# Kernel tuning notes

Measured on AMD Instinct MI355X. Metric: run time of the kernel, lower is better.

## Reference

```python
import jax, jax.numpy as jnp
import numpy as np

G = 5000      # n_genes (nodes)
IN = 64       # in_dim
D = 128       # embed_dims
E = 240000    # edges (before self-loops)
SLOPE = 0.2   # leakyrelu_slope (outer) and GATv2 internal negative_slope (PyG default 0.2)


def setup_inputs() -> dict:
    key = jax.random.key(0)
    ks = jax.random.split(key, 12)
    s = 0.05
    return {
        "x": jax.random.normal(ks[0], (G, IN), jnp.float32),
        "edge_index": jax.random.randint(ks[1], (2, E), 0, G, jnp.int64),
        # per-gene input linears: n_genes independent Linear(in_dim -> embed_dims)
        "W_in": jax.random.normal(ks[2], (G, IN, D), jnp.float32) * s,
        "b_in": jnp.zeros((G, D), jnp.float32),
        # GATv2Conv params (heads=1): lin_l, lin_r, att, bias
        "W_l": jax.random.normal(ks[3], (D, D), jnp.float32) * s,
        "b_l": jnp.zeros((D,), jnp.float32),
        "W_r": jax.random.normal(ks[4], (D, D), jnp.float32) * s,
        "b_r": jnp.zeros((D,), jnp.float32),
        "att": jax.random.normal(ks[5], (D,), jnp.float32) * s,
        "bias": jnp.zeros((D,), jnp.float32),
        # output MLP: Linear(D*G -> D), Linear(D -> 1)
        "W1": jax.random.normal(ks[6], (D * G, D), jnp.float32) * 0.001,
        "b1": jnp.zeros((D,), jnp.float32),
        "W2": jax.random.normal(ks[7], (D, 1), jnp.float32) * s,
        "b2": jnp.zeros((1,), jnp.float32),
    }


def _leaky(v, slope):
    return jnp.where(v >= 0, v, slope * v)


def reference(x, edge_index, W_in, b_in, W_l, b_l, W_r, b_r, att, bias, W1, b1, W2, b2):
    # per-gene linear + relu: [G, IN] x [G, IN, D] -> [G, D]
    h = jax.nn.relu(jnp.einsum("gi,gid->gd", x, W_in) + b_in)

    # GATv2Conv (heads=1, concat, add_self_loops=True)
    xl = h @ W_l + b_l  # source-side transform [G, D]
    xr = h @ W_r + b_r  # target-side transform [G, D]
    loop = jnp.arange(G, dtype=edge_index.dtype)
    src = jnp.concatenate([edge_index[0], loop])  # [E+G]
    dst = jnp.concatenate([edge_index[1], loop])

    # attention logits per edge: att . LeakyReLU(xl[src] + xr[dst])
    e = _leaky(xl[src] + xr[dst], 0.2) @ att  # [E+G]

    # segment softmax over edges sharing a destination
    m = jax.ops.segment_max(e, dst, num_segments=G)  # [G]
    w = jnp.exp(e - m[dst])
    z = jax.ops.segment_sum(w, dst, num_segments=G)  # [G]
    alpha = w / z[dst]  # every node has a self-loop, z > 0

    # scatter-aggregate weighted messages
    out = jax.ops.segment_sum(alpha[:, None] * xl[src], dst, num_segments=G) + bias  # [G, D]

    out = _leaky(out, SLOPE)
    flat = out.reshape(-1)  # [G*D]
    h1 = jax.nn.relu(flat @ W1 + b1)
    return h1 @ W2 + b2  # [1]
```

## Files before the change

### kernel.cpp

```cpp
#include <hip/hip_runtime.h>
#include <math.h>

#define G 5000
#define IN 64
#define D 128
#define E 240000
#define EG (E + G)
#define SLOPE 0.2f
#define GD (G * D)
#define CAP 128
#define NB_M 1250
#define NB_PG 1250
#define NB_H 240
#define NB_X 1250

__device__ __forceinline__ float leaky(float v) { return v >= 0.f ? v : SLOPE * v; }

__global__ __launch_bounds__(256) void k_fuseA(const float* __restrict__ x,
                                               const float* __restrict__ Win,
                                               const float* __restrict__ bin,
                                               float* __restrict__ h,
                                               const int* __restrict__ srcA,
                                               const int* __restrict__ dstA,
                                               int* __restrict__ cnt,
                                               int* __restrict__ ssrc,
                                               float* __restrict__ outz) {
    if (blockIdx.x == 0 && threadIdx.x == 0) *outz = 0.f;
    if (blockIdx.x < NB_PG) {
        int g = (blockIdx.x * 256 + threadIdx.x) >> 6;
        int lane = threadIdx.x & 63;
        if (g >= G) return;
        float xv = x[g * IN + lane];
        const float* W = Win + (size_t)g * IN * D + lane * 2;
        float2 acc = *(const float2*)(bin + g * D + lane * 2);
#pragma unroll
        for (int i = 0; i < IN; ++i) {
            float xi = __shfl(xv, i);
            float2 w2 = *(const float2*)(W + (size_t)i * D);
            acc.x = fmaf(xi, w2.x, acc.x);
            acc.y = fmaf(xi, w2.y, acc.y);
        }
        float2 o = { fmaxf(acc.x, 0.f), fmaxf(acc.y, 0.f) };
        *(float2*)(h + g * D + lane * 2) = o;
    } else {
        int base = ((blockIdx.x - NB_PG) * 256 + threadIdx.x) * 4;
        if (base >= EG) return;
        if (base + 4 <= E) {
            int4 s4 = *(const int4*)(srcA + base);
            int4 d4 = *(const int4*)(dstA + base);
            int p;
            p = atomicAdd(&cnt[d4.x], 1); if (p < CAP) ssrc[d4.x * CAP + p] = s4.x;
            p = atomicAdd(&cnt[d4.y], 1); if (p < CAP) ssrc[d4.y * CAP + p] = s4.y;
            p = atomicAdd(&cnt[d4.z], 1); if (p < CAP) ssrc[d4.z * CAP + p] = s4.z;
            p = atomicAdd(&cnt[d4.w], 1); if (p < CAP) ssrc[d4.w * CAP + p] = s4.w;
        } else {
            for (int kk = 0; kk < 4; ++kk) {
                int i = base + kk;
                if (i < EG) {
                    int s, t;
                    if (i < E) { s = srcA[i]; t = dstA[i]; }
                    else { s = i - E; t = s; }
                    int p = atomicAdd(&cnt[t], 1);
                    if (p < CAP) ssrc[t * CAP + p] = s;
                }
            }
        }
    }
}

__global__ __launch_bounds__(256) void k_xlxr3(const float* __restrict__ h,
                                               const float* __restrict__ Wl,
                                               const float* __restrict__ bl,
                                               const float* __restrict__ Wr,
                                               const float* __restrict__ br,
                                               float* __restrict__ xl,
                                               float* __restrict__ xr) {
    int g0 = blockIdx.x * 4;
    int tid = threadIdx.x;
    int half = tid >> 7;
    int col = tid & 127;
    const float* W = half ? Wr : Wl;
    const float* bb = half ? br : bl;
    float* o = half ? xr : xl;
    const float* h0p = h + (size_t)(g0 + 0) * D;
    const float* h1p = h + (size_t)(g0 + 1) * D;
    const float* h2p = h + (size_t)(g0 + 2) * D;
    const float* h3p = h + (size_t)(g0 + 3) * D;
    float b = bb[col];
    float acc0 = b, acc1 = b, acc2 = b, acc3 = b;
#pragma unroll 8
    for (int k4 = 0; k4 < 32; ++k4) {
        int k = k4 * 4;
        float4 hv0 = *(const float4*)(h0p + k);
        float4 hv1 = *(const float4*)(h1p + k);
        float4 hv2 = *(const float4*)(h2p + k);
        float4 hv3 = *(const float4*)(h3p + k);
        float w0 = W[(size_t)(k + 0) * D + col];
        float w1 = W[(size_t)(k + 1) * D + col];
        float w2 = W[(size_t)(k + 2) * D + col];
        float w3 = W[(size_t)(k + 3) * D + col];
        acc0 = fmaf(hv0.x, w0, acc0); acc0 = fmaf(hv0.y, w1, acc0);
        acc0 = fmaf(hv0.z, w2, acc0); acc0 = fmaf(hv0.w, w3, acc0);
        acc1 = fmaf(hv1.x, w0, acc1); acc1 = fmaf(hv1.y, w1, acc1);
        acc1 = fmaf(hv1.z, w2, acc1); acc1 = fmaf(hv1.w, w3, acc1);
        acc2 = fmaf(hv2.x, w0, acc2); acc2 = fmaf(hv2.y, w1, acc2);
        acc2 = fmaf(hv2.z, w2, acc2); acc2 = fmaf(hv2.w, w3, acc2);
        acc3 = fmaf(hv3.x, w0, acc3); acc3 = fmaf(hv3.y, w1, acc3);
        acc3 = fmaf(hv3.z, w2, acc3); acc3 = fmaf(hv3.w, w3, acc3);
    }
    o[(size_t)(g0 + 0) * D + col] = acc0;
    o[(size_t)(g0 + 1) * D + col] = acc1;
    o[(size_t)(g0 + 2) * D + col] = acc2;
    o[(size_t)(g0 + 3) * D + col] = acc3;
}

__global__ __launch_bounds__(256) void k_aggmlp(const int* __restrict__ cnt,
                                                const int* __restrict__ ssrc,
                                                const float* __restrict__ xl,
                                                const float* __restrict__ xr,
                                                const float* __restrict__ att,
                                                const float* __restrict__ bias,
                                                const float* __restrict__ W1,
                                                float* __restrict__ partials) {
    int wid = threadIdx.x >> 6;
    int lane = threadIdx.x & 63;
    int t = __builtin_amdgcn_readfirstlane(blockIdx.x * 4 + wid);
    __shared__ float w_lds[4][64];
    __shared__ int   s_lds[4][64];
    __shared__ float2 red[4][64];
    const float* xrt = xr + (size_t)t * D;
    int lane2 = lane * 2;
    int deg = cnt[t]; if (deg > CAP) deg = CAP;
    const int* srow = ssrc + t * CAP;
    float2 acc = { 0.f, 0.f };
    float z = 0.f;
    for (int base = 0; base < deg; base += 64) {
        int nv = deg - base; if (nv > 64) nv = 64;
        int mye = base + lane;
        int s = srow[mye < deg ? mye : deg - 1];
        const float* xls = xl + (size_t)s * D;
        float v0 = 0.f, v1 = 0.f;
#pragma unroll
        for (int dc = 0; dc < D; dc += 8) {
            float4 xa = *(const float4*)(xls + dc);
            float4 xb = *(const float4*)(xls + dc + 4);
            float4 ra = *(const float4*)(xrt + dc);
            float4 rb = *(const float4*)(xrt + dc + 4);
            float4 aa = *(const float4*)(att + dc);
            float4 ab = *(const float4*)(att + dc + 4);
            v0 = fmaf(aa.x, leaky(xa.x + ra.x), v0);
            v0 = fmaf(aa.y, leaky(xa.y + ra.y), v0);
            v0 = fmaf(aa.z, leaky(xa.z + ra.z), v0);
            v0 = fmaf(aa.w, leaky(xa.w + ra.w), v0);
            v1 = fmaf(ab.x, leaky(xb.x + rb.x), v1);
            v1 = fmaf(ab.y, leaky(xb.y + rb.y), v1);
            v1 = fmaf(ab.z, leaky(xb.z + rb.z), v1);
            v1 = fmaf(ab.w, leaky(xb.w + rb.w), v1);
        }
        float w = (lane < nv) ? expf(v0 + v1) : 0.f;
        z += w;
        w_lds[wid][lane] = w;
        s_lds[wid][lane] = s;
        for (int e = 0; e < nv; e += 4) {
            float4 w4 = *(const float4*)&w_lds[wid][e];
            int4   s4 = *(const int4*)&s_lds[wid][e];
            float2 l0 = *(const float2*)(xl + (size_t)s4.x * D + lane2);
            float2 l1 = *(const float2*)(xl + (size_t)s4.y * D + lane2);
            float2 l2 = *(const float2*)(xl + (size_t)s4.z * D + lane2);
            float2 l3 = *(const float2*)(xl + (size_t)s4.w * D + lane2);
            acc.x = fmaf(w4.x, l0.x, acc.x); acc.y = fmaf(w4.x, l0.y, acc.y);
            acc.x = fmaf(w4.y, l1.x, acc.x); acc.y = fmaf(w4.y, l1.y, acc.y);
            acc.x = fmaf(w4.z, l2.x, acc.x); acc.y = fmaf(w4.z, l2.y, acc.y);
            acc.x = fmaf(w4.w, l3.x, acc.x); acc.y = fmaf(w4.w, l3.y, acc.y);
        }
    }
#pragma unroll
    for (int off = 32; off; off >>= 1) z += __shfl_xor(z, off);
    float inv = 1.f / z;
    float2 bv = *(const float2*)(bias + lane2);
    float2 o = { leaky(acc.x * inv + bv.x), leaky(acc.y * inv + bv.y) };

    const float* W1p = W1 + (size_t)t * D * D + lane2;
    float2 m = { 0.f, 0.f };
#pragma unroll 8
    for (int dp = 0; dp < 64; ++dp) {
        float fx = __shfl(o.x, dp);
        float fy = __shfl(o.y, dp);
        float2 wa = *(const float2*)(W1p + (size_t)(2 * dp) * D);
        float2 wb = *(const float2*)(W1p + (size_t)(2 * dp + 1) * D);
        m.x = fmaf(fx, wa.x, m.x); m.y = fmaf(fx, wa.y, m.y);
        m.x = fmaf(fy, wb.x, m.x); m.y = fmaf(fy, wb.y, m.y);
    }
    red[wid][lane] = m;
    __syncthreads();
    if (wid == 0) {
        float2 s0 = red[0][lane], s1 = red[1][lane], s2 = red[2][lane], s3 = red[3][lane];
        float2 s = { s0.x + s1.x + s2.x + s3.x, s0.y + s1.y + s2.y + s3.y };
        *(float2*)(partials + (size_t)blockIdx.x * D + lane2) = s;
    }
}

__global__ __launch_bounds__(1024) void k_final8(const float* __restrict__ partials,
                                                 const float* __restrict__ b1,
                                                 const float* __restrict__ W2,
                                                 const float* __restrict__ b2,
                                                 float* __restrict__ out) {
    int tid = threadIdx.x;
    int rg = tid >> 4;
    int cl = tid & 15;
    int c = blockIdx.x * 16 + cl;
    float s = 0.f;
    for (int r = rg; r < NB_M; r += 64) s += partials[(size_t)r * D + c];
    __shared__ float red[64][16];
    red[rg][cl] = s;
    __syncthreads();
    if (tid < 128) {
        int cc = tid & 15, seg = tid >> 4;
        float t2 = red[seg * 8][cc];
        for (int m = 1; m < 8; ++m) t2 += red[seg * 8 + m][cc];
        red[seg * 8][cc] = t2;
    }
    __syncthreads();
    if (tid < 16) {
        float tot = 0.f;
        for (int m = 0; m < 8; ++m) tot += red[m * 8][tid];
        float h1 = fmaxf(tot + b1[blockIdx.x * 16 + tid], 0.f);
        red[0][tid] = h1 * W2[blockIdx.x * 16 + tid];
    }
    __syncthreads();
    if (tid == 0) {
        float o = 0.f;
        for (int m = 0; m < 16; ++m) o += red[0][m];
        if (blockIdx.x == 0) o += b2[0];
        atomicAdd(out, o);
    }
}

extern "C" void kernel_launch(void* const* d_in, const int* in_sizes, int n_in,
                              void* d_out, int out_size, void* d_ws, size_t ws_size,
                              hipStream_t stream) {
    const float* x    = (const float*)d_in[0];
    const int*   ei   = (const int*)d_in[1];
    const float* Win  = (const float*)d_in[2];
    const float* bin  = (const float*)d_in[3];
    const float* Wl   = (const float*)d_in[4];
    const float* bl   = (const float*)d_in[5];
    const float* Wr   = (const float*)d_in[6];
    const float* br   = (const float*)d_in[7];
    const float* att  = (const float*)d_in[8];
    const float* bias = (const float*)d_in[9];
    const float* W1   = (const float*)d_in[10];
    const float* b1   = (const float*)d_in[11];
    const float* W2   = (const float*)d_in[12];
    const float* b2   = (const float*)d_in[13];
    float* out = (float*)d_out;

    float* ws       = (float*)d_ws;
    float* h        = ws;
    float* xl       = h  + GD;
    float* xr       = xl + GD;
    float* partials = xr + GD;
    int*   ssrc     = (int*)(partials + (size_t)NB_M * D);
    int*   cnt      = ssrc + (size_t)G * CAP;

    const int* srcA = ei;
    const int* dstA = ei + E;

    hipMemsetAsync(cnt, 0, G * sizeof(int), stream);
    k_fuseA<<<NB_PG + NB_H, 256, 0, stream>>>(x, Win, bin, h, srcA, dstA, cnt, ssrc, out);
    k_xlxr3<<<NB_X, 256, 0, stream>>>(h, Wl, bl, Wr, br, xl, xr);
    k_aggmlp<<<NB_M, 256, 0, stream>>>(cnt, ssrc, xl, xr, att, bias, W1, partials);
    k_final8<<<8, 1024, 0, stream>>>(partials, b1, W2, b2, out);
}
```

Measured before the change: 154.8 us.

## Compute attention logits cooperatively per edge, reusing gathered xl rows for aggregation

Replaces the lane-per-edge logit computation (each lane reads a full 128-float xl row) with a wave-cooperative scheme: each lane holds two feature columns, the four edges' rows are gathered once, and the logits come from a cross-lane butterfly reduction. The same gathered xl values then feed the weighted aggregation, so each source row is read once instead of twice and the LDS staging is removed. The cost is more shuffle reductions per edge (six steps for each of four edges) and redundant exp evaluation across all lanes. The kernel is likely bound by gather traffic, which this change halves.

```diff
diff --git a/kernel.cpp b/kernel.cpp
--- a/kernel.cpp
+++ b/kernel.cpp
@@ -125,57 +125,55 @@
     int wid = threadIdx.x >> 6;
     int lane = threadIdx.x & 63;
     int t = __builtin_amdgcn_readfirstlane(blockIdx.x * 4 + wid);
-    __shared__ float w_lds[4][64];
-    __shared__ int   s_lds[4][64];
     __shared__ float2 red[4][64];
-    const float* xrt = xr + (size_t)t * D;
     int lane2 = lane * 2;
+    float2 a  = *(const float2*)(att + lane2);
+    float2 r2 = *(const float2*)(xr + (size_t)t * D + lane2);
     int deg = cnt[t]; if (deg > CAP) deg = CAP;
     const int* srow = ssrc + t * CAP;
     float2 acc = { 0.f, 0.f };
     float z = 0.f;
     for (int base = 0; base < deg; base += 64) {
         int nv = deg - base; if (nv > 64) nv = 64;
-        int mye = base + lane;
-        int s = srow[mye < deg ? mye : deg - 1];
-        const float* xls = xl + (size_t)s * D;
-        float v0 = 0.f, v1 = 0.f;
+        int sv = srow[base + (lane < nv ? lane : nv - 1)];
+        int e = 0;
+        for (; e + 4 <= nv; e += 4) {
+            int s0 = __shfl(sv, e), s1 = __shfl(sv, e + 1);
+            int s2 = __shfl(sv, e + 2), s3 = __shfl(sv, e + 3);
+            float2 l0 = *(const float2*)(xl + (size_t)s0 * D + lane2);
+            float2 l1 = *(const float2*)(xl + (size_t)s1 * D + lane2);
+            float2 l2 = *(const float2*)(xl + (size_t)s2 * D + lane2);
+            float2 l3 = *(const float2*)(xl + (size_t)s3 * D + lane2);
+            float v0 = leaky(l0.x + r2.x) * a.x + leaky(l0.y + r2.y) * a.y;
+            float v1 = leaky(l1.x + r2.x) * a.x + leaky(l1.y + r2.y) * a.y;
+            float v2 = leaky(l2.x + r2.x) * a.x + leaky(l2.y + r2.y) * a.y;
+            float v3 = leaky(l3.x + r2.x) * a.x + leaky(l3.y + r2.y) * a.y;
 #pragma unroll
-        for (int dc = 0; dc < D; dc += 8) {
-            float4 xa = *(const float4*)(xls + dc);
-            float4 xb = *(const float4*)(xls + dc + 4);
-            float4 ra = *(const float4*)(xrt + dc);
-            float4 rb = *(const float4*)(xrt + dc + 4);
-            float4 aa = *(const float4*)(att + dc);
-            float4 ab = *(const float4*)(att + dc + 4);
-            v0 = fmaf(aa.x, leaky(xa.x + ra.x), v0);
-            v0 = fmaf(aa.y, leaky(xa.y + ra.y), v0);
-            v0 = fmaf(aa.z, leaky(xa.z + ra.z), v0);
-            v0 = fmaf(aa.w, leaky(xa.w + ra.w), v0);
-            v1 = fmaf(ab.x, leaky(xb.x + rb.x), v1);
-            v1 = fmaf(ab.y, leaky(xb.y + rb.y), v1);
-            v1 = fmaf(ab.z, leaky(xb.z + rb.z), v1);
-            v1 = fmaf(ab.w, leaky(xb.w + rb.w), v1);
-        }
-        float w = (lane < nv) ? expf(v0 + v1) : 0.f;
-        z += w;
-        w_lds[wid][lane] = w;
-        s_lds[wid][lane] = s;
-        for (int e = 0; e < nv; e += 4) {
-            float4 w4 = *(const float4*)&w_lds[wid][e];
-            int4   s4 = *(const int4*)&s_lds[wid][e];
-            float2 l0 = *(const float2*)(xl + (size_t)s4.x * D + lane2);
-            float2 l1 = *(const float2*)(xl + (size_t)s4.y * D + lane2);
-            float2 l2 = *(const float2*)(xl + (size_t)s4.z * D + lane2);
-            float2 l3 = *(const float2*)(xl + (size_t)s4.w * D + lane2);
-            acc.x = fmaf(w4.x, l0.x, acc.x); acc.y = fmaf(w4.x, l0.y, acc.y);
-            acc.x = fmaf(w4.y, l1.x, acc.x); acc.y = fmaf(w4.y, l1.y, acc.y);
-            acc.x = fmaf(w4.z, l2.x, acc.x); acc.y = fmaf(w4.z, l2.y, acc.y);
-            acc.x = fmaf(w4.w, l3.x, acc.x); acc.y = fmaf(w4.w, l3.y, acc.y);
-        }
-    }
+            for (int off = 32; off; off >>= 1) {
+                v0 += __shfl_xor(v0, off);
+                v1 += __shfl_xor(v1, off);
+                v2 += __shfl_xor(v2, off);
+                v3 += __shfl_xor(v3, off);
+            }
+            float w0 = expf(v0), w1 = expf(v1), w2 = expf(v2), w3 = expf(v3);
+            z += (w0 + w1) + (w2 + w3);
+            acc.x = fmaf(w0, l0.x, acc.x); acc.y = fmaf(w0, l0.y, acc.y);
+            acc.x = fmaf(w1, l1.x, acc.x); acc.y = fmaf(w1, l1.y, acc.y);
+            acc.x = fmaf(w2, l2.x, acc.x); acc.y = fmaf(w2, l2.y, acc.y);
+            acc.x = fmaf(w3, l3.x, acc.x); acc.y = fmaf(w3, l3.y, acc.y);
+        }
+        for (; e < nv; ++e) {
+            int s = __shfl(sv, e);
+            float2 l = *(const float2*)(xl + (size_t)s * D + lane2);
+            float v = leaky(l.x + r2.x) * a.x + leaky(l.y + r2.y) * a.y;
 #pragma unroll
-    for (int off = 32; off; off >>= 1) z += __shfl_xor(z, off);
+            for (int off = 32; off; off >>= 1) v += __shfl_xor(v, off);
+            float w = expf(v);
+            z += w;
+            acc.x = fmaf(w, l.x, acc.x);
+            acc.y = fmaf(w, l.y, acc.y);
+        }
+    }
     float inv = 1.f / z;
     float2 bv = *(const float2*)(bias + lane2);
     float2 o = { leaky(acc.x * inv + bv.x), leaky(acc.y * inv + bv.y) };
```

Result: faster. 140.9 us (-9.0%).
